# Optimization experiments

Measured on AMD Instinct MI355X. Metric: run time of the kernel, lower is better.

Reference implementation:

```python
import jax, jax.numpy as jnp
import numpy as np

B, Q, H = 32, 1024, 1024
HR = H // 2          # reduced hidden size (reduction_factor=2)
C = 4096             # codebook size (num_tokens)
COMMIT_W = 0.25


def setup_inputs() -> dict:
    key = jax.random.key(0)
    ks = jax.random.split(key, 10)
    s = lambda fan: 1.0 / np.sqrt(fan)
    return {
        "x": jax.random.normal(ks[0], (B, Q, H), dtype=jnp.float32),
        # encoder: Linear(H,H) -> ReLU -> Linear(H,HR)
        "enc_w1": jax.random.normal(ks[1], (H, H), jnp.float32) * s(H),
        "enc_b1": jnp.zeros((H,), jnp.float32),
        "enc_w2": jax.random.normal(ks[2], (H, HR), jnp.float32) * s(H),
        "enc_b2": jnp.zeros((HR,), jnp.float32),
        # codebook: [C, HR]
        "codebook": jax.random.normal(ks[3], (C, HR), jnp.float32),
        # decoder: Linear(HR,H) -> ReLU -> Linear(H,H)
        "dec_w1": jax.random.normal(ks[4], (HR, H), jnp.float32) * s(HR),
        "dec_b1": jnp.zeros((H,), jnp.float32),
        "dec_w2": jax.random.normal(ks[5], (H, H), jnp.float32) * s(H),
        "dec_b2": jnp.zeros((H,), jnp.float32),
    }


def reference(x, enc_w1, enc_b1, enc_w2, enc_b2, codebook,
              dec_w1, dec_b1, dec_w2, dec_b2):
    # prepare_input = Identity (normalize=False)
    # encoder MLP
    h = jax.nn.relu(jnp.einsum("bqh,hk->bqk", x, enc_w1) + enc_b1)
    z = jnp.einsum("bqh,hr->bqr", h, enc_w2) + enc_b2          # [B,Q,HR] pre-quant

    # nearest-codebook search: argmin_c ||z - e_c||^2 (expand, skip z^2 term)
    zf = z.reshape(-1, HR)                                      # [N,HR]
    d = (jnp.sum(codebook * codebook, axis=-1)[None, :]
         - 2.0 * zf @ codebook.T)                               # [N,C]
    idx = jnp.argmin(d, axis=-1)                                # [N]
    quantized = codebook[idx].reshape(B, Q, HR)                 # gather lookup

    # straight-through estimator + commitment loss
    quantized_st = z + jax.lax.stop_gradient(quantized - z)
    commit_loss = COMMIT_W * jnp.mean(
        (z - jax.lax.stop_gradient(quantized)) ** 2)

    # decoder MLP
    h2 = jax.nn.relu(jnp.einsum("bqr,rh->bqh", quantized_st, dec_w1) + dec_b1)
    recon = jnp.einsum("bqh,hk->bqk", h2, dec_w2) + dec_b2      # [B,Q,H]

    token_indices = idx.reshape(B, Q)
    return recon, quantized_st, token_indices, commit_loss
```

## Files before the change

kernel.cpp:

```cpp
#include <hip/hip_runtime.h>


#define BM 128
#define BN 128
#define BK 16
#define TM 8
#define TN 8

#define NROW 32768
#define HDIM 1024
#define HRDIM 512
#define CODES 4096

__global__ __launch_bounds__(256) void sgemm_bias(
    const float* __restrict__ A, const float* __restrict__ B,
    const float* __restrict__ bias, float* __restrict__ C,
    int M, int N, int K, int do_relu)
{
    __shared__ __align__(16) float As[BK][BM + 4];
    __shared__ __align__(16) float Bs[BK][BN + 4];

    const int tid = threadIdx.x;
    const int tx = tid & 15;
    const int ty = tid >> 4;
    const int block_row = blockIdx.y * BM;
    const int block_col = blockIdx.x * BN;

    float acc[TM][TN] = {};

    const int a_r0 = tid >> 2;
    const int a_c0 = (tid & 3) << 2;
    const int b_r0 = tid >> 5;
    const int b_c0 = (tid & 31) << 2;

    const float* Ab = A + (size_t)block_row * K;

    for (int k0 = 0; k0 < K; k0 += BK) {
#pragma unroll
        for (int i = 0; i < 2; ++i) {
            int r = a_r0 + i * 64;
            float4 v = *(const float4*)(Ab + (size_t)r * K + k0 + a_c0);
            As[a_c0 + 0][r] = v.x;
            As[a_c0 + 1][r] = v.y;
            As[a_c0 + 2][r] = v.z;
            As[a_c0 + 3][r] = v.w;
        }
#pragma unroll
        for (int i = 0; i < 2; ++i) {
            int r = b_r0 + i * 8;
            float4 v = *(const float4*)(B + (size_t)(k0 + r) * N + block_col + b_c0);
            *(float4*)(&Bs[r][b_c0]) = v;
        }
        __syncthreads();
#pragma unroll
        for (int k = 0; k < BK; ++k) {
            float4 a0 = *(const float4*)(&As[k][ty * 8]);
            float4 a1 = *(const float4*)(&As[k][ty * 8 + 4]);
            float4 b0 = *(const float4*)(&Bs[k][tx * 4]);
            float4 b1 = *(const float4*)(&Bs[k][tx * 4 + 64]);
            float am[TM] = {a0.x, a0.y, a0.z, a0.w, a1.x, a1.y, a1.z, a1.w};
            float bn[TN] = {b0.x, b0.y, b0.z, b0.w, b1.x, b1.y, b1.z, b1.w};
#pragma unroll
            for (int i = 0; i < TM; ++i)
#pragma unroll
                for (int j = 0; j < TN; ++j)
                    acc[i][j] = fmaf(am[i], bn[j], acc[i][j]);
        }
        __syncthreads();
    }

    float4 bv0 = *(const float4*)(bias + block_col + tx * 4);
    float4 bv1 = *(const float4*)(bias + block_col + 64 + tx * 4);
#pragma unroll
    for (int i = 0; i < TM; ++i) {
        int gr = block_row + ty * TM + i;
        float* Crow = C + (size_t)gr * N + block_col;
        float4 v0, v1;
        v0.x = acc[i][0] + bv0.x;  v0.y = acc[i][1] + bv0.y;
        v0.z = acc[i][2] + bv0.z;  v0.w = acc[i][3] + bv0.w;
        v1.x = acc[i][4] + bv1.x;  v1.y = acc[i][5] + bv1.y;
        v1.z = acc[i][6] + bv1.z;  v1.w = acc[i][7] + bv1.w;
        if (do_relu) {
            v0.x = fmaxf(v0.x, 0.0f); v0.y = fmaxf(v0.y, 0.0f);
            v0.z = fmaxf(v0.z, 0.0f); v0.w = fmaxf(v0.w, 0.0f);
            v1.x = fmaxf(v1.x, 0.0f); v1.y = fmaxf(v1.y, 0.0f);
            v1.z = fmaxf(v1.z, 0.0f); v1.w = fmaxf(v1.w, 0.0f);
        }
        *(float4*)(Crow + tx * 4) = v0;
        *(float4*)(Crow + 64 + tx * 4) = v1;
    }
}

__global__ __launch_bounds__(256) void cb2_kernel(const float* __restrict__ CB,
                                                  float* __restrict__ cb2)
{
    int row = blockIdx.x * 4 + (threadIdx.x >> 6);
    int lane = threadIdx.x & 63;
    const float* cr = CB + (size_t)row * HRDIM;
    float s = 0.0f;
#pragma unroll
    for (int i = 0; i < 2; ++i) {
        int c = lane * 4 + i * 256;
        float4 v = *(const float4*)(cr + c);
        s = fmaf(v.x, v.x, s);
        s = fmaf(v.y, v.y, s);
        s = fmaf(v.z, v.z, s);
        s = fmaf(v.w, v.w, s);
    }
#pragma unroll
    for (int off = 32; off > 0; off >>= 1) s += __shfl_down(s, off, 64);
    if (lane == 0) cb2[row] = s;
}

__device__ __forceinline__ unsigned int float_orderkey(float f)
{
    unsigned int u = __float_as_uint(f);
    return (u & 0x80000000u) ? ~u : (u | 0x80000000u);
}

__global__ __launch_bounds__(256) void dist_argmin(
    const float* __restrict__ Z, const float* __restrict__ CB,
    const float* __restrict__ cb2, unsigned long long* __restrict__ packed)
{
    __shared__ __align__(16) float As[BK][BM + 4];
    __shared__ __align__(16) float Bs[BK][BN + 4];

    const int tid = threadIdx.x;
    const int tx = tid & 15;
    const int ty = tid >> 4;
    const int block_row = blockIdx.y * BM;
    const int block_col = blockIdx.x * BN;
    const int K = HRDIM;

    float acc[TM][TN] = {};

    const int a_r0 = tid >> 2;
    const int a_c0 = (tid & 3) << 2;

    const float* Ab = Z + (size_t)block_row * K;

    for (int k0 = 0; k0 < K; k0 += BK) {
#pragma unroll
        for (int i = 0; i < 2; ++i) {
            int r = a_r0 + i * 64;
            float4 v = *(const float4*)(Ab + (size_t)r * K + k0 + a_c0);
            As[a_c0 + 0][r] = v.x;
            As[a_c0 + 1][r] = v.y;
            As[a_c0 + 2][r] = v.z;
            As[a_c0 + 3][r] = v.w;
        }
#pragma unroll
        for (int i = 0; i < 2; ++i) {
            int n = a_r0 + i * 64;
            float4 v = *(const float4*)(CB + (size_t)(block_col + n) * K + k0 + a_c0);
            Bs[a_c0 + 0][n] = v.x;
            Bs[a_c0 + 1][n] = v.y;
            Bs[a_c0 + 2][n] = v.z;
            Bs[a_c0 + 3][n] = v.w;
        }
        __syncthreads();
#pragma unroll
        for (int k = 0; k < BK; ++k) {
            float4 a0 = *(const float4*)(&As[k][ty * 8]);
            float4 a1 = *(const float4*)(&As[k][ty * 8 + 4]);
            float4 b0 = *(const float4*)(&Bs[k][tx * 4]);
            float4 b1 = *(const float4*)(&Bs[k][tx * 4 + 64]);
            float am[TM] = {a0.x, a0.y, a0.z, a0.w, a1.x, a1.y, a1.z, a1.w};
            float bn[TN] = {b0.x, b0.y, b0.z, b0.w, b1.x, b1.y, b1.z, b1.w};
#pragma unroll
            for (int i = 0; i < TM; ++i)
#pragma unroll
                for (int j = 0; j < TN; ++j)
                    acc[i][j] = fmaf(am[i], bn[j], acc[i][j]);
        }
        __syncthreads();
    }

    float4 c2a = *(const float4*)(cb2 + block_col + tx * 4);
    float4 c2b = *(const float4*)(cb2 + block_col + 64 + tx * 4);
    const float c2[TN] = {c2a.x, c2a.y, c2a.z, c2a.w, c2b.x, c2b.y, c2b.z, c2b.w};

#pragma unroll
    for (int i = 0; i < TM; ++i) {
        unsigned long long best = 0xFFFFFFFFFFFFFFFFull;
#pragma unroll
        for (int j = 0; j < TN; ++j) {
            int col = block_col + ((j < 4) ? (tx * 4 + j) : (64 + tx * 4 + j - 4));
            float d = c2[j] - 2.0f * acc[i][j];
            unsigned long long p =
                ((unsigned long long)float_orderkey(d) << 32) | (unsigned int)col;
            best = (p < best) ? p : best;
        }
#pragma unroll
        for (int m = 1; m < 16; m <<= 1) {
            unsigned long long o = __shfl_xor(best, m, 64);
            best = (o < best) ? o : best;
        }
        if (tx == 0)
            atomicMin(&packed[block_row + ty * TM + i], best);
    }
}

__global__ __launch_bounds__(256) void gather_pass(
    const float* __restrict__ Z, const unsigned long long* __restrict__ packed,
    const float* __restrict__ CB, float* __restrict__ Q,
    float* __restrict__ IDX, float* __restrict__ partials)
{
    __shared__ float s[4];
    int row = blockIdx.x * 4 + (threadIdx.x >> 6);
    int lane = threadIdx.x & 63;

    unsigned long long p = packed[row];
    int idx = (int)(unsigned int)(p & 0xFFFFFFFFull);

    const float* zr = Z + (size_t)row * HRDIM;
    const float* cr = CB + (size_t)idx * HRDIM;
    float* qr = Q + (size_t)row * HRDIM;

    float z2 = 0.0f;
#pragma unroll
    for (int i = 0; i < 2; ++i) {
        int c = lane * 4 + i * 256;
        float4 zv = *(const float4*)(zr + c);
        float4 cv = *(const float4*)(cr + c);
        *(float4*)(qr + c) = cv;
        z2 = fmaf(zv.x, zv.x, z2);
        z2 = fmaf(zv.y, zv.y, z2);
        z2 = fmaf(zv.z, zv.z, z2);
        z2 = fmaf(zv.w, zv.w, z2);
    }
#pragma unroll
    for (int off = 32; off > 0; off >>= 1) z2 += __shfl_down(z2, off, 64);

    if (lane == 0) {
        unsigned int u = (unsigned int)(p >> 32);
        unsigned int bits = (u & 0x80000000u) ? (u ^ 0x80000000u) : ~u;
        float dmin = __uint_as_float(bits);
        IDX[row] = (float)idx;
        s[threadIdx.x >> 6] = z2 + dmin;
    }
    __syncthreads();
    if (threadIdx.x == 0) partials[blockIdx.x] = s[0] + s[1] + s[2] + s[3];
}

__global__ __launch_bounds__(256) void commit_final(
    const float* __restrict__ partials, int n, float* __restrict__ outv)
{
    __shared__ float s[256];
    float v = 0.0f;
    for (int i = threadIdx.x; i < n; i += 256) v += partials[i];
    s[threadIdx.x] = v;
    __syncthreads();
    for (int st = 128; st > 0; st >>= 1) {
        if (threadIdx.x < st) s[threadIdx.x] += s[threadIdx.x + st];
        __syncthreads();
    }
    if (threadIdx.x == 0)
        outv[0] = 0.25f * s[0] / (float)(NROW * HRDIM);
}

extern "C" void kernel_launch(void* const* d_in, const int* in_sizes, int n_in,
                              void* d_out, int out_size, void* d_ws, size_t ws_size,
                              hipStream_t stream)
{
    const float* x   = (const float*)d_in[0];
    const float* ew1 = (const float*)d_in[1];
    const float* eb1 = (const float*)d_in[2];
    const float* ew2 = (const float*)d_in[3];
    const float* eb2 = (const float*)d_in[4];
    const float* cb  = (const float*)d_in[5];
    const float* dw1 = (const float*)d_in[6];
    const float* db1 = (const float*)d_in[7];
    const float* dw2 = (const float*)d_in[8];
    const float* db2 = (const float*)d_in[9];

    float* out   = (float*)d_out;
    float* recon = out;
    float* qst   = out + 33554432;
    float* idxf  = out + 33554432 + 16777216;
    float* loss  = out + 33554432 + 16777216 + 32768;

    char* ws = (char*)d_ws;
    float* h = (float*)ws;
    unsigned long long* packed =
        (unsigned long long*)(ws + (size_t)134217728);
    float* cb2      = (float*)(ws + (size_t)134217728 + 262144);
    float* partials = (float*)(ws + (size_t)134217728 + 262144 + 16384);
    float* z = recon;

    hipMemsetAsync(packed, 0xFF, NROW * sizeof(unsigned long long), stream);
    cb2_kernel<<<CODES / 4, 256, 0, stream>>>(cb, cb2);

    sgemm_bias<<<dim3(HDIM / BN, NROW / BM), 256, 0, stream>>>(
        x, ew1, eb1, h, NROW, HDIM, HDIM, 1);
    sgemm_bias<<<dim3(HRDIM / BN, NROW / BM), 256, 0, stream>>>(
        h, ew2, eb2, z, NROW, HRDIM, HDIM, 0);

    dist_argmin<<<dim3(CODES / BN, NROW / BM), 256, 0, stream>>>(z, cb, cb2, packed);
    gather_pass<<<NROW / 4, 256, 0, stream>>>(z, packed, cb, qst, idxf, partials);

    sgemm_bias<<<dim3(HDIM / BN, NROW / BM), 256, 0, stream>>>(
        qst, dw1, db1, h, NROW, HDIM, HRDIM, 1);
    sgemm_bias<<<dim3(HDIM / BN, NROW / BM), 256, 0, stream>>>(
        h, dw2, db2, recon, NROW, HDIM, HDIM, 0);

    commit_final<<<1, 256, 0, stream>>>(partials, NROW / 4, loss);
}
```

Baseline: 3.913 ms.

## Replace fp32 distance argmin with bf16 MFMA coarse pass plus fp32 recheck

The fp32 SIMT distance GEMM is split into two stages. First, z and the codebook are converted to bf16 and a matrix-core (MFMA) pass writes a per-row minimum for each group of 32 codes. Then an fp32 recheck evaluates exact distances only for groups whose coarse minimum lies within an error bound derived from the norms. This removes most of the fp32 FLOPs of the 32768x4096x512 search but adds conversion passes, a localmin buffer and a per-row recheck kernel whose cost depends on how many groups pass the threshold. The threshold margin is a heuristic, so an argmin could in principle be missed.

Measured after the change: 4.001 ms. 1.02x slower.

```diff
diff --git a/kernel.cpp b/kernel.cpp
--- a/kernel.cpp
+++ b/kernel.cpp
@@ -11,6 +11,9 @@
 #define HDIM 1024
 #define HRDIM 512
 #define CODES 4096
+
+typedef __attribute__((ext_vector_type(8))) short bf16x8;
+typedef __attribute__((ext_vector_type(4))) float f32x4;
 
 __global__ __launch_bounds__(256) void sgemm_bias(
     const float* __restrict__ A, const float* __restrict__ B,
@@ -92,7 +95,8 @@
 }
 
 __global__ __launch_bounds__(256) void cb2_kernel(const float* __restrict__ CB,
-                                                  float* __restrict__ cb2)
+                                                  float* __restrict__ cb2,
+                                                  unsigned int* __restrict__ cb2max)
 {
     int row = blockIdx.x * 4 + (threadIdx.x >> 6);
     int lane = threadIdx.x & 63;
@@ -109,7 +113,117 @@
     }
 #pragma unroll
     for (int off = 32; off > 0; off >>= 1) s += __shfl_down(s, off, 64);
-    if (lane == 0) cb2[row] = s;
+    if (lane == 0) {
+        cb2[row] = s;
+        atomicMax(cb2max, __float_as_uint(s));
+    }
+}
+
+__device__ __forceinline__ unsigned short f2bf(float f)
+{
+    unsigned int u = __float_as_uint(f);
+    return (unsigned short)((u + 0x7FFFu + ((u >> 16) & 1u)) >> 16);
+}
+
+__global__ __launch_bounds__(256) void to_bf16(const float* __restrict__ in,
+                                               unsigned short* __restrict__ out,
+                                               int nvec)
+{
+    int i = blockIdx.x * 256 + threadIdx.x;
+    if (i >= nvec) return;
+    float4 a = ((const float4*)in)[2 * i];
+    float4 b = ((const float4*)in)[2 * i + 1];
+    ushort4 o0, o1;
+    o0.x = f2bf(a.x); o0.y = f2bf(a.y); o0.z = f2bf(a.z); o0.w = f2bf(a.w);
+    o1.x = f2bf(b.x); o1.y = f2bf(b.y); o1.z = f2bf(b.z); o1.w = f2bf(b.w);
+    ((ushort4*)out)[2 * i] = o0;
+    ((ushort4*)out)[2 * i + 1] = o1;
+}
+
+__global__ __launch_bounds__(256) void coarse_dist(
+    const unsigned short* __restrict__ Zh, const unsigned short* __restrict__ CBh,
+    const float* __restrict__ cb2, float* __restrict__ localmin)
+{
+    __shared__ __align__(16) unsigned short As[128 * 64];
+    __shared__ __align__(16) unsigned short Bs[128 * 64];
+    __shared__ __align__(16) float sm[128][4];
+
+    const int tid = threadIdx.x;
+    const int lane = tid & 63;
+    const int w = tid >> 6;
+    const int wr = w >> 1, wc = w & 1;
+    const int block_row = blockIdx.y * 128;
+    const int block_col = blockIdx.x * 128;
+
+    f32x4 acc[4][4] = {};
+
+    for (int k0 = 0; k0 < HRDIM; k0 += 64) {
+#pragma unroll
+        for (int i = 0; i < 4; ++i) {
+            int e = (tid + i * 256) * 8;
+            int r = e >> 6;
+            int c = e & 63;
+            int addr = (r * 128 + c * 2) ^ ((r & 7) << 4);
+            uint4 va = *(const uint4*)(Zh + (size_t)(block_row + r) * HRDIM + k0 + c);
+            *(uint4*)((char*)As + addr) = va;
+            uint4 vb = *(const uint4*)(CBh + (size_t)(block_col + r) * HRDIM + k0 + c);
+            *(uint4*)((char*)Bs + addr) = vb;
+        }
+        __syncthreads();
+#pragma unroll
+        for (int kk = 0; kk < 2; ++kk) {
+            bf16x8 af[4], bfr[4];
+#pragma unroll
+            for (int m = 0; m < 4; ++m) {
+                int R = wr * 64 + m * 16 + (lane & 15);
+                int byte = (R * 128 + (kk * 32 + (lane >> 4) * 8) * 2) ^ ((R & 7) << 4);
+                af[m] = *(const bf16x8*)((const char*)As + byte);
+            }
+#pragma unroll
+            for (int n = 0; n < 4; ++n) {
+                int R = wc * 64 + n * 16 + (lane & 15);
+                int byte = (R * 128 + (kk * 32 + (lane >> 4) * 8) * 2) ^ ((R & 7) << 4);
+                bfr[n] = *(const bf16x8*)((const char*)Bs + byte);
+            }
+#pragma unroll
+            for (int m = 0; m < 4; ++m)
+#pragma unroll
+                for (int n = 0; n < 4; ++n)
+                    acc[m][n] = __builtin_amdgcn_mfma_f32_16x16x32_bf16(
+                        af[m], bfr[n], acc[m][n], 0, 0, 0);
+        }
+        __syncthreads();
+    }
+
+    float c2[4];
+#pragma unroll
+    for (int n = 0; n < 4; ++n)
+        c2[n] = cb2[block_col + wc * 64 + n * 16 + (lane & 15)];
+
+#pragma unroll
+    for (int m = 0; m < 4; ++m) {
+#pragma unroll
+        for (int g = 0; g < 2; ++g) {
+#pragma unroll
+            for (int q = 0; q < 4; ++q) {
+                float d0 = c2[g * 2 + 0] - 2.0f * acc[m][g * 2 + 0][q];
+                float d1 = c2[g * 2 + 1] - 2.0f * acc[m][g * 2 + 1][q];
+                float v = fminf(d0, d1);
+#pragma unroll
+                for (int msk = 1; msk < 16; msk <<= 1)
+                    v = fminf(v, __shfl_xor(v, msk, 64));
+                if ((lane & 15) == 0) {
+                    int rl = wr * 64 + m * 16 + (lane >> 4) * 4 + q;
+                    sm[rl][wc * 2 + g] = v;
+                }
+            }
+        }
+    }
+    __syncthreads();
+    if (tid < 128) {
+        float4 v4 = *(const float4*)(&sm[tid][0]);
+        *(float4*)(localmin + (size_t)(block_row + tid) * 128 + (block_col >> 5)) = v4;
+    }
 }
 
 __device__ __forceinline__ unsigned int float_orderkey(float f)
@@ -118,86 +232,85 @@
     return (u & 0x80000000u) ? ~u : (u | 0x80000000u);
 }
 
-__global__ __launch_bounds__(256) void dist_argmin(
+__global__ __launch_bounds__(256) void recheck(
     const float* __restrict__ Z, const float* __restrict__ CB,
-    const float* __restrict__ cb2, unsigned long long* __restrict__ packed)
-{
-    __shared__ __align__(16) float As[BK][BM + 4];
-    __shared__ __align__(16) float Bs[BK][BN + 4];
-
+    const float* __restrict__ cb2, const float* __restrict__ localmin,
+    const unsigned int* __restrict__ cb2max,
+    unsigned long long* __restrict__ packed)
+{
+    __shared__ __align__(16) float zs[HRDIM];
+    __shared__ float lm[128];
+    __shared__ float red[8];
+    __shared__ unsigned long long bred[4];
+
+    const int row = blockIdx.x;
     const int tid = threadIdx.x;
-    const int tx = tid & 15;
-    const int ty = tid >> 4;
-    const int block_row = blockIdx.y * BM;
-    const int block_col = blockIdx.x * BN;
-    const int K = HRDIM;
-
-    float acc[TM][TN] = {};
-
-    const int a_r0 = tid >> 2;
-    const int a_c0 = (tid & 3) << 2;
-
-    const float* Ab = Z + (size_t)block_row * K;
-
-    for (int k0 = 0; k0 < K; k0 += BK) {
-#pragma unroll
-        for (int i = 0; i < 2; ++i) {
-            int r = a_r0 + i * 64;
-            float4 v = *(const float4*)(Ab + (size_t)r * K + k0 + a_c0);
-            As[a_c0 + 0][r] = v.x;
-            As[a_c0 + 1][r] = v.y;
-            As[a_c0 + 2][r] = v.z;
-            As[a_c0 + 3][r] = v.w;
-        }
-#pragma unroll
-        for (int i = 0; i < 2; ++i) {
-            int n = a_r0 + i * 64;
-            float4 v = *(const float4*)(CB + (size_t)(block_col + n) * K + k0 + a_c0);
-            Bs[a_c0 + 0][n] = v.x;
-            Bs[a_c0 + 1][n] = v.y;
-            Bs[a_c0 + 2][n] = v.z;
-            Bs[a_c0 + 3][n] = v.w;
-        }
-        __syncthreads();
-#pragma unroll
-        for (int k = 0; k < BK; ++k) {
-            float4 a0 = *(const float4*)(&As[k][ty * 8]);
-            float4 a1 = *(const float4*)(&As[k][ty * 8 + 4]);
-            float4 b0 = *(const float4*)(&Bs[k][tx * 4]);
-            float4 b1 = *(const float4*)(&Bs[k][tx * 4 + 64]);
-            float am[TM] = {a0.x, a0.y, a0.z, a0.w, a1.x, a1.y, a1.z, a1.w};
-            float bn[TN] = {b0.x, b0.y, b0.z, b0.w, b1.x, b1.y, b1.z, b1.w};
-#pragma unroll
-            for (int i = 0; i < TM; ++i)
-#pragma unroll
-                for (int j = 0; j < TN; ++j)
-                    acc[i][j] = fmaf(am[i], bn[j], acc[i][j]);
-        }
-        __syncthreads();
-    }
-
-    float4 c2a = *(const float4*)(cb2 + block_col + tx * 4);
-    float4 c2b = *(const float4*)(cb2 + block_col + 64 + tx * 4);
-    const float c2[TN] = {c2a.x, c2a.y, c2a.z, c2a.w, c2b.x, c2b.y, c2b.z, c2b.w};
-
-#pragma unroll
-    for (int i = 0; i < TM; ++i) {
-        unsigned long long best = 0xFFFFFFFFFFFFFFFFull;
-#pragma unroll
-        for (int j = 0; j < TN; ++j) {
-            int col = block_col + ((j < 4) ? (tx * 4 + j) : (64 + tx * 4 + j - 4));
-            float d = c2[j] - 2.0f * acc[i][j];
-            unsigned long long p =
-                ((unsigned long long)float_orderkey(d) << 32) | (unsigned int)col;
-            best = (p < best) ? p : best;
-        }
-#pragma unroll
-        for (int m = 1; m < 16; m <<= 1) {
-            unsigned long long o = __shfl_xor(best, m, 64);
-            best = (o < best) ? o : best;
-        }
-        if (tx == 0)
-            atomicMin(&packed[block_row + ty * TM + i], best);
+
+    float2 zv = ((const float2*)(Z + (size_t)row * HRDIM))[tid];
+    ((float2*)zs)[tid] = zv;
+    float z2p = zv.x * zv.x + zv.y * zv.y;
+#pragma unroll
+    for (int off = 32; off > 0; off >>= 1) z2p += __shfl_down(z2p, off, 64);
+
+    float lmv = 1e30f;
+    if (tid < 128) {
+        lmv = localmin[(size_t)row * 128 + tid];
+        lm[tid] = lmv;
+    }
+#pragma unroll
+    for (int off = 32; off > 0; off >>= 1)
+        lmv = fminf(lmv, __shfl_down(lmv, off, 64));
+    if ((tid & 63) == 0) {
+        red[tid >> 6] = z2p;
+        red[4 + (tid >> 6)] = lmv;
+    }
+    __syncthreads();
+    const float z2 = red[0] + red[1] + red[2] + red[3];
+    const float m = fminf(fminf(red[4], red[5]), fminf(red[6], red[7]));
+    const float thr = m + 0.05f * sqrtf(z2 * __uint_as_float(*cb2max)) + 0.01f;
+
+    const int col_in_g = tid >> 3;
+    const int sub = tid & 7;
+    unsigned long long best = 0xFFFFFFFFFFFFFFFFull;
+
+    for (int g = 0; g < 128; ++g) {
+        if (lm[g] <= thr) {
+            int c = g * 32 + col_in_g;
+            const float4* cbp = (const float4*)(CB + (size_t)c * HRDIM) + sub * 16;
+            const float4* zp = (const float4*)zs + sub * 16;
+            float dot = 0.0f;
+#pragma unroll
+            for (int j = 0; j < 16; ++j) {
+                float4 cv = cbp[j];
+                float4 zq = zp[j];
+                dot = fmaf(cv.x, zq.x, dot);
+                dot = fmaf(cv.y, zq.y, dot);
+                dot = fmaf(cv.z, zq.z, dot);
+                dot = fmaf(cv.w, zq.w, dot);
+            }
+#pragma unroll
+            for (int off = 4; off > 0; off >>= 1) dot += __shfl_down(dot, off, 64);
+            if (sub == 0) {
+                float d = cb2[c] - 2.0f * dot;
+                unsigned long long p =
+                    ((unsigned long long)float_orderkey(d) << 32) | (unsigned int)c;
+                best = (p < best) ? p : best;
+            }
+        }
+    }
+#pragma unroll
+    for (int off = 32; off > 0; off >>= 1) {
+        unsigned long long o = __shfl_down(best, off, 64);
+        best = (o < best) ? o : best;
+    }
+    if ((tid & 63) == 0) bred[tid >> 6] = best;
+    __syncthreads();
+    if (tid == 0) {
+        unsigned long long b = bred[0];
+        b = (bred[1] < b) ? bred[1] : b;
+        b = (bred[2] < b) ? bred[2] : b;
+        b = (bred[3] < b) ? bred[3] : b;
+        packed[row] = b;
     }
 }
 
@@ -282,21 +395,32 @@
 
     char* ws = (char*)d_ws;
     float* h = (float*)ws;
+    unsigned short* zh  = (unsigned short*)ws;
+    unsigned short* cbh = (unsigned short*)(ws + (size_t)33554432);
+    float* localmin = (float*)(ws + (size_t)37748736);
     unsigned long long* packed =
         (unsigned long long*)(ws + (size_t)134217728);
     float* cb2      = (float*)(ws + (size_t)134217728 + 262144);
     float* partials = (float*)(ws + (size_t)134217728 + 262144 + 16384);
+    unsigned int* cb2max =
+        (unsigned int*)(ws + (size_t)134217728 + 262144 + 16384 + 32768);
     float* z = recon;
 
-    hipMemsetAsync(packed, 0xFF, NROW * sizeof(unsigned long long), stream);
-    cb2_kernel<<<CODES / 4, 256, 0, stream>>>(cb, cb2);
+    hipMemsetAsync(cb2max, 0, 4, stream);
+    cb2_kernel<<<CODES / 4, 256, 0, stream>>>(cb, cb2, cb2max);
 
     sgemm_bias<<<dim3(HDIM / BN, NROW / BM), 256, 0, stream>>>(
         x, ew1, eb1, h, NROW, HDIM, HDIM, 1);
     sgemm_bias<<<dim3(HRDIM / BN, NROW / BM), 256, 0, stream>>>(
         h, ew2, eb2, z, NROW, HRDIM, HDIM, 0);
 
-    dist_argmin<<<dim3(CODES / BN, NROW / BM), 256, 0, stream>>>(z, cb, cb2, packed);
+    to_bf16<<<(NROW * HRDIM / 8 + 255) / 256, 256, 0, stream>>>(
+        z, zh, NROW * HRDIM / 8);
+    to_bf16<<<(CODES * HRDIM / 8 + 255) / 256, 256, 0, stream>>>(
+        cb, cbh, CODES * HRDIM / 8);
+    coarse_dist<<<dim3(CODES / 128, NROW / 128), 256, 0, stream>>>(
+        zh, cbh, cb2, localmin);
+    recheck<<<NROW, 256, 0, stream>>>(z, cb, cb2, localmin, cb2max, packed);
     gather_pass<<<NROW / 4, 256, 0, stream>>>(z, packed, cb, qst, idxf, partials);
 
     sgemm_bias<<<dim3(HDIM / BN, NROW / BM), 256, 0, stream>>>(
```
